# Performance work log

Hardware: AMD Instinct MI355X
Metric: run time of the kernel (lower is better)

Reference implementation:

```python
import jax, jax.numpy as jnp
import numpy as np

CUTOFF = 5.5
R0 = CUTOFF
R1 = CUTOFF * 4.0 / 5.0
SIGMA2 = 0.5 ** 2
N_ATOMS = 20000
CN_LIST = jnp.arange(16, dtype=jnp.float32)  # KDE bin centers

S, E = 8, 1_000_000


def setup_inputs() -> dict:
    key = jax.random.key(0)
    k1, k2 = jax.random.split(key)
    # pair displacement vectors, scaled so distances span the switching region
    neighbor_vectors = jax.random.normal(k1, (S, E, 3), dtype=jnp.float32) * 2.5
    first_atom = jax.random.randint(k2, (S, E), 0, N_ATOMS, dtype=jnp.int32)
    return {"neighbor_vectors": neighbor_vectors, "first_atom": first_atom}


def f_coord(y):
    # switching function: 1 for y<=0, 0 for y>=1, (y-1)^2 (1+2y) between
    mid = (y - 1.0) ** 2 * (1.0 + 2.0 * y)
    return jnp.where(y <= 0.0, 1.0, jnp.where(y >= 1.0, 0.0, mid))


def reference(neighbor_vectors, first_atom):
    s, e, _ = neighbor_vectors.shape
    distances = jnp.linalg.norm(neighbor_vectors, axis=-1)          # [S,E]
    z = f_coord((distances - R1) / (R0 - R1))                        # [S,E]
    # per-system scatter-add of z onto atoms -> coordination numbers
    flat_idx = (first_atom + jnp.arange(s, dtype=jnp.int32)[:, None] * N_ATOMS).reshape(-1)
    coords = jax.ops.segment_sum(z.reshape(-1), flat_idx, num_segments=s * N_ATOMS)
    coords = coords.reshape(s, N_ATOMS)                              # [S,N]
    # Gaussian KDE histogram over cn bins, summed over atoms
    diff = coords[:, :, None] - CN_LIST[None, None, :]               # [S,N,K]
    cn_histo = jnp.exp(-diff * diff * (0.5 / SIGMA2)).sum(axis=1)    # [S,K]
    return cn_histo
```

## Files before the change

### kernel.cpp

```cpp
#include <hip/hip_runtime.h>

static constexpr int S_SYS   = 8;
static constexpr int E_PAIRS = 1000000;
static constexpr int N_A     = 20000;
static constexpr int NBINS   = 16;
static constexpr int BPS     = 32;
static constexpr int BLK     = 1024;
static constexpr int UNR     = 2;
static constexpr float SCALE   = 4194304.0f;
static constexpr float INV_SCL = 1.0f / 4194304.0f;
static constexpr float INV11 = 1.0f / 1.1f;

typedef unsigned u32x4 __attribute__((ext_vector_type(4)));

__global__ __launch_bounds__(BLK, 4) void coord_lds_u32(
    const float* __restrict__ vec, const int* __restrict__ atom,
    unsigned* __restrict__ partial)
{
    __shared__ __align__(16) unsigned lc[N_A];
    for (int i = threadIdx.x; i < N_A; i += BLK) lc[i] = 0u;
    __syncthreads();

    const int s = blockIdx.y;
    const int Q = E_PAIRS / 4;
    const float4* vb = reinterpret_cast<const float4*>(vec) + (size_t)s * Q * 3;
    const int4*   ib = reinterpret_cast<const int4*>(atom) + (size_t)s * Q;

    const int W = BPS * BLK;
    for (int t = blockIdx.x * BLK + threadIdx.x; t < Q; t += W * UNR) {
        float4 A[UNR], B[UNR], C[UNR];
        int4   id[UNR];
        bool   ok[UNR];
        #pragma unroll
        for (int u = 0; u < UNR; ++u) {
            int tq = t + u * W;
            ok[u] = (tq < Q);
            if (ok[u]) {
                A[u] = vb[3 * tq]; B[u] = vb[3 * tq + 1]; C[u] = vb[3 * tq + 2];
                id[u] = ib[tq];
            }
        }
        #pragma unroll
        for (int u = 0; u < UNR; ++u) {
            if (!ok[u]) continue;
            float px[4] = {A[u].x, A[u].w, B[u].z, C[u].y};
            float py[4] = {A[u].y, B[u].x, B[u].w, C[u].z};
            float pz[4] = {A[u].z, B[u].y, C[u].x, C[u].w};
            int ids[4]  = {id[u].x, id[u].y, id[u].z, id[u].w};
            #pragma unroll
            for (int j = 0; j < 4; ++j) {
                float q = px[j]*px[j] + py[j]*py[j] + pz[j]*pz[j];
                float d = sqrtf(q);
                float y = (d - 4.4f) * INV11;
                y = fminf(fmaxf(y, 0.0f), 1.0f);
                float uu = y - 1.0f;
                float z = uu * uu * (1.0f + 2.0f * y);
                atomicAdd(&lc[ids[j]], __float2uint_rn(z * SCALE));
            }
        }
    }
    __syncthreads();

    u32x4* po = reinterpret_cast<u32x4*>(partial + ((size_t)s * BPS + blockIdx.x) * N_A);
    const u32x4* ls = reinterpret_cast<const u32x4*>(lc);
    for (int i = threadIdx.x; i < N_A / 4; i += BLK)
        __builtin_nontemporal_store(ls[i], &po[i]);
}

__global__ __launch_bounds__(256) void kde_reduce_u32(
    const unsigned* __restrict__ partial, float* __restrict__ out)
{
    int s = blockIdx.y;
    int a = blockIdx.x * 256 + threadIdx.x;
    bool valid = (a < N_A);

    unsigned acc = 0u;
    if (valid) {
        const unsigned* p = partial + (size_t)s * BPS * N_A + a;
        #pragma unroll 8
        for (int b = 0; b < BPS; ++b)
            acc += __builtin_nontemporal_load(&p[(size_t)b * N_A]);
    }
    float c = (float)acc * INV_SCL;

    float vals[NBINS];
    #pragma unroll
    for (int k = 0; k < NBINS; ++k) {
        float d = c - (float)k;
        vals[k] = valid ? expf(-2.0f * d * d) : 0.0f;
    }

    #pragma unroll
    for (int k = 0; k < NBINS; ++k) {
        #pragma unroll
        for (int off = 32; off > 0; off >>= 1)
            vals[k] += __shfl_down(vals[k], off, 64);
    }

    __shared__ float sbin[4][NBINS];
    int wave = threadIdx.x >> 6;
    int lane = threadIdx.x & 63;
    if (lane == 0) {
        #pragma unroll
        for (int k = 0; k < NBINS; ++k) sbin[wave][k] = vals[k];
    }
    __syncthreads();
    if (threadIdx.x < NBINS) {
        float v = sbin[0][threadIdx.x] + sbin[1][threadIdx.x]
                + sbin[2][threadIdx.x] + sbin[3][threadIdx.x];
        unsafeAtomicAdd(&out[s * NBINS + threadIdx.x], v);
    }
}

__global__ __launch_bounds__(256) void coord_scatter(
    const float* __restrict__ vec, const int* __restrict__ atom,
    float* __restrict__ coords)
{
    const int P4 = S_SYS * E_PAIRS / 4;
    int stride = gridDim.x * blockDim.x;
    for (int t = blockIdx.x * blockDim.x + threadIdx.x; t < P4; t += stride) {
        const float4* v4 = reinterpret_cast<const float4*>(vec) + 3ull * (unsigned)t;
        float4 A = v4[0], B = v4[1], C = v4[2];
        int4 id = reinterpret_cast<const int4*>(atom)[t];
        int s = (t * 4) / E_PAIRS;
        float* cs = coords + s * N_A;
        float px[4] = {A.x, A.w, B.z, C.y};
        float py[4] = {A.y, B.x, B.w, C.z};
        float pz[4] = {A.z, B.y, C.x, C.w};
        int ids[4]  = {id.x, id.y, id.z, id.w};
        #pragma unroll
        for (int j = 0; j < 4; ++j) {
            float d = sqrtf(px[j]*px[j] + py[j]*py[j] + pz[j]*pz[j]);
            float y = (d - 4.4f) / 1.1f;
            float z;
            if (y <= 0.0f)      z = 1.0f;
            else if (y >= 1.0f) z = 0.0f;
            else { float u = y - 1.0f; z = u * u * (1.0f + 2.0f * y); }
            if (z != 0.0f) unsafeAtomicAdd(&cs[ids[j]], z);
        }
    }
}

__global__ __launch_bounds__(256) void kde_reduce_f32(
    const float* __restrict__ coords, float* __restrict__ out)
{
    int s = blockIdx.y;
    int a = blockIdx.x * 256 + threadIdx.x;
    bool valid = (a < N_A);
    float c = valid ? coords[(size_t)s * N_A + a] : 0.0f;

    float vals[NBINS];
    #pragma unroll
    for (int k = 0; k < NBINS; ++k) {
        float d = c - (float)k;
        vals[k] = valid ? expf(-2.0f * d * d) : 0.0f;
    }
    #pragma unroll
    for (int k = 0; k < NBINS; ++k) {
        #pragma unroll
        for (int off = 32; off > 0; off >>= 1)
            vals[k] += __shfl_down(vals[k], off, 64);
    }
    __shared__ float sbin[4][NBINS];
    int wave = threadIdx.x >> 6;
    int lane = threadIdx.x & 63;
    if (lane == 0) {
        #pragma unroll
        for (int k = 0; k < NBINS; ++k) sbin[wave][k] = vals[k];
    }
    __syncthreads();
    if (threadIdx.x < NBINS) {
        float v = sbin[0][threadIdx.x] + sbin[1][threadIdx.x]
                + sbin[2][threadIdx.x] + sbin[3][threadIdx.x];
        unsafeAtomicAdd(&out[s * NBINS + threadIdx.x], v);
    }
}

extern "C" void kernel_launch(void* const* d_in, const int* in_sizes, int n_in,
                              void* d_out, int out_size, void* d_ws, size_t ws_size,
                              hipStream_t stream) {
    const float* vec  = (const float*)d_in[0];
    const int*   atom = (const int*)d_in[1];
    float* out = (float*)d_out;

    (void)hipMemsetAsync(out, 0, (size_t)S_SYS * NBINS * sizeof(float), stream);

    const size_t need = (size_t)S_SYS * BPS * N_A * sizeof(unsigned);
    dim3 g2((N_A + 255) / 256, S_SYS);

    if (ws_size >= need) {
        unsigned* ws = (unsigned*)d_ws;
        dim3 g1(BPS, S_SYS);
        coord_lds_u32<<<g1, BLK, 0, stream>>>(vec, atom, ws);
        kde_reduce_u32<<<g2, 256, 0, stream>>>(ws, out);
    } else {
        float* ws = (float*)d_ws;
        (void)hipMemsetAsync(ws, 0, (size_t)S_SYS * N_A * sizeof(float), stream);
        coord_scatter<<<2048, 256, 0, stream>>>(vec, atom, ws);
        kde_reduce_f32<<<g2, 256, 0, stream>>>(ws, out);
    }
}
```

Baseline: 41.02 us.

## Pack per-block coordination partials to 16-bit and fold output zeroing into scatter kernel

Lowers the fixed-point scale so each block's per-atom partial sums fit in 16 bits, packing two atoms per 32-bit word. This halves the intermediate workspace written by the scatter kernel and read by the reduce kernel, which now handles two atoms per thread. The separate memset of the output is replaced by zeroing inside the first kernel, and sqrtf becomes the raw hardware builtin. The cost is coarser fixed-point precision and a risk of 16-bit overflow if an atom receives many pairs within one block.

```diff
diff --git a/kernel.cpp b/kernel.cpp
--- a/kernel.cpp
+++ b/kernel.cpp
@@ -7,21 +7,24 @@
 static constexpr int BPS     = 32;
 static constexpr int BLK     = 1024;
 static constexpr int UNR     = 2;
-static constexpr float SCALE   = 4194304.0f;
-static constexpr float INV_SCL = 1.0f / 4194304.0f;
+static constexpr float SCALE   = 1024.0f;
+static constexpr float INV_SCL = 1.0f / 1024.0f;
 static constexpr float INV11 = 1.0f / 1.1f;
 
 typedef unsigned u32x4 __attribute__((ext_vector_type(4)));
 
 __global__ __launch_bounds__(BLK, 4) void coord_lds_u32(
     const float* __restrict__ vec, const int* __restrict__ atom,
-    unsigned* __restrict__ partial)
+    unsigned short* __restrict__ partial, float* __restrict__ out)
 {
     __shared__ __align__(16) unsigned lc[N_A];
     for (int i = threadIdx.x; i < N_A; i += BLK) lc[i] = 0u;
-    __syncthreads();
 
     const int s = blockIdx.y;
+    if (blockIdx.x == 0 && threadIdx.x < NBINS)
+        out[s * NBINS + threadIdx.x] = 0.0f;
+    __syncthreads();
+
     const int Q = E_PAIRS / 4;
     const float4* vb = reinterpret_cast<const float4*>(vec) + (size_t)s * Q * 3;
     const int4*   ib = reinterpret_cast<const int4*>(atom) + (size_t)s * Q;
@@ -50,7 +53,7 @@
             #pragma unroll
             for (int j = 0; j < 4; ++j) {
                 float q = px[j]*px[j] + py[j]*py[j] + pz[j]*pz[j];
-                float d = sqrtf(q);
+                float d = __builtin_amdgcn_sqrtf(q);
                 float y = (d - 4.4f) * INV11;
                 y = fminf(fmaxf(y, 0.0f), 1.0f);
                 float uu = y - 1.0f;
@@ -62,32 +65,40 @@
     __syncthreads();
 
     u32x4* po = reinterpret_cast<u32x4*>(partial + ((size_t)s * BPS + blockIdx.x) * N_A);
-    const u32x4* ls = reinterpret_cast<const u32x4*>(lc);
-    for (int i = threadIdx.x; i < N_A / 4; i += BLK)
-        __builtin_nontemporal_store(ls[i], &po[i]);
-}
-
-__global__ __launch_bounds__(256) void kde_reduce_u32(
-    const unsigned* __restrict__ partial, float* __restrict__ out)
+    for (int i = threadIdx.x; i < N_A / 8; i += BLK) {
+        u32x4 v;
+        #pragma unroll
+        for (int k = 0; k < 4; ++k)
+            v[k] = (lc[8 * i + 2 * k] & 0xFFFFu) | (lc[8 * i + 2 * k + 1] << 16);
+        __builtin_nontemporal_store(v, &po[i]);
+    }
+}
+
+__global__ __launch_bounds__(256) void kde_reduce_u16(
+    const unsigned* __restrict__ partial32, float* __restrict__ out)
 {
     int s = blockIdx.y;
-    int a = blockIdx.x * 256 + threadIdx.x;
-    bool valid = (a < N_A);
-
-    unsigned acc = 0u;
+    int a0 = blockIdx.x * 512 + 2 * threadIdx.x;
+    bool valid = (a0 < N_A);
+
+    unsigned acc0 = 0u, acc1 = 0u;
     if (valid) {
-        const unsigned* p = partial + (size_t)s * BPS * N_A + a;
+        const unsigned* p = partial32 + ((size_t)s * BPS * N_A + a0) / 2;
         #pragma unroll 8
-        for (int b = 0; b < BPS; ++b)
-            acc += __builtin_nontemporal_load(&p[(size_t)b * N_A]);
-    }
-    float c = (float)acc * INV_SCL;
+        for (int b = 0; b < BPS; ++b) {
+            unsigned v = __builtin_nontemporal_load(&p[(size_t)b * (N_A / 2)]);
+            acc0 += v & 0xFFFFu;
+            acc1 += v >> 16;
+        }
+    }
+    float c0 = (float)acc0 * INV_SCL;
+    float c1 = (float)acc1 * INV_SCL;
 
     float vals[NBINS];
     #pragma unroll
     for (int k = 0; k < NBINS; ++k) {
-        float d = c - (float)k;
-        vals[k] = valid ? expf(-2.0f * d * d) : 0.0f;
+        float d0 = c0 - (float)k, d1 = c1 - (float)k;
+        vals[k] = valid ? (expf(-2.0f * d0 * d0) + expf(-2.0f * d1 * d1)) : 0.0f;
     }
 
     #pragma unroll
@@ -183,20 +194,20 @@
     const int*   atom = (const int*)d_in[1];
     float* out = (float*)d_out;
 
-    (void)hipMemsetAsync(out, 0, (size_t)S_SYS * NBINS * sizeof(float), stream);
-
-    const size_t need = (size_t)S_SYS * BPS * N_A * sizeof(unsigned);
-    dim3 g2((N_A + 255) / 256, S_SYS);
+    const size_t need = (size_t)S_SYS * BPS * N_A * sizeof(unsigned short);
 
     if (ws_size >= need) {
-        unsigned* ws = (unsigned*)d_ws;
+        unsigned short* ws = (unsigned short*)d_ws;
         dim3 g1(BPS, S_SYS);
-        coord_lds_u32<<<g1, BLK, 0, stream>>>(vec, atom, ws);
-        kde_reduce_u32<<<g2, 256, 0, stream>>>(ws, out);
+        coord_lds_u32<<<g1, BLK, 0, stream>>>(vec, atom, ws, out);
+        dim3 g2((N_A + 511) / 512, S_SYS);
+        kde_reduce_u16<<<g2, 256, 0, stream>>>((const unsigned*)ws, out);
     } else {
         float* ws = (float*)d_ws;
+        (void)hipMemsetAsync(out, 0, (size_t)S_SYS * NBINS * sizeof(float), stream);
         (void)hipMemsetAsync(ws, 0, (size_t)S_SYS * N_A * sizeof(float), stream);
         coord_scatter<<<2048, 256, 0, stream>>>(vec, atom, ws);
-        kde_reduce_f32<<<g2, 256, 0, stream>>>(ws, out);
-    }
-}
+        dim3 g2f((N_A + 255) / 256, S_SYS);
+        kde_reduce_f32<<<g2f, 256, 0, stream>>>(ws, out);
+    }
+}
```

After: 33.74 us. -17.7%, faster.
